# Kernel optimization log

Hardware: AMD Instinct MI355X
Metric: run time of the kernel (lower is better)

The kernel has to match this reference:

```python
import jax, jax.numpy as jnp
import numpy as np

S_VIEWS = 7  # sampled_view from init


def _select_idx(F0, s_views):
    # F0: [B, N, C]; returns idx: [B, s_views] int32 view indices
    B, N, C = F0.shape
    # argmax over views per channel (torch.max(F0,1)[1]) -> [B, C], values in [0, N)
    f_max = jnp.argmax(F0, axis=1)
    # bounded histogram over the N view bins (replaces torch.unique(..., return_counts=True))
    counts = jnp.zeros((B, N), jnp.int32).at[jnp.arange(B)[:, None], f_max].add(1)
    u = jnp.sum(counts > 0, axis=-1)  # number of unique views per batch, [B]
    # --- topk branch (u >= s_views) ---
    # torch.unique is ascending, so topk-by-count with ascending tie-break ==
    # lax.top_k over the per-bin counts (ties -> lower bin index == smaller view id)
    _, idx_topk = jax.lax.top_k(counts, s_views)  # [B, s_views]
    # --- replication-pad branch (u < s_views) ---
    # sorted unique view ids first, sentinel N for empty bins
    sorted_views = jnp.sort(jnp.where(counts > 0, jnp.arange(N)[None, :], N), axis=-1)
    # left-pad with the smallest unique value: position j maps to max(j-(s-u), 0)
    pad_pos = jnp.maximum(jnp.arange(s_views)[None, :] - (s_views - u[:, None]), 0)
    idx_pad = jnp.take_along_axis(sorted_views, pad_pos, axis=-1)  # [B, s_views]
    return jnp.where((u < s_views)[:, None], idx_pad, idx_topk).astype(jnp.int32)


def setup_inputs() -> dict:
    key = jax.random.key(0)
    k1, k2 = jax.random.split(key)
    B, N, C = 256, 20, 4096
    F0 = jax.random.normal(k1, (B, N, C), dtype=jnp.float32)
    vertices0 = jax.random.normal(k2, (B, N, 3), dtype=jnp.float32)
    return {"F0": F0, "vertices0": vertices0, "k": 7}


def reference(F0, vertices0, k):
    idx = _select_idx(F0, S_VIEWS)  # [B, s_views]
    F_new = jnp.take_along_axis(F0, idx[:, :, None], axis=1)          # [B, s_views, C]
    vertices_new = jnp.take_along_axis(vertices0, idx[:, :, None], axis=1)  # [B, s_views, 3]
    return (F_new, vertices_new)
```

## Files before the change

### kernel.cpp

```cpp
#include <hip/hip_runtime.h>

#define BATCHES  256
#define NVIEWS   20
#define CHANNELS 4096
#define KSEL     7
#define NT       1024

__global__ __launch_bounds__(NT) void view_select_kernel(
    const float* __restrict__ F0,
    const float* __restrict__ V0,
    float* __restrict__ out)
{
    const int b = blockIdx.x;
    const int t = threadIdx.x;

    __shared__ int counts[NVIEWS];
    __shared__ int sidx[KSEL];

    if (t < NVIEWS) counts[t] = 0;
    __syncthreads();

    const float* Fb = F0 + (size_t)b * NVIEWS * CHANNELS;
    const float4* Fb4 = (const float4*)Fb;

    float4 best = Fb4[t];
    int bi0 = 0, bi1 = 0, bi2 = 0, bi3 = 0;
    #pragma unroll
    for (int n = 1; n < NVIEWS; ++n) {
        float4 v = Fb4[(size_t)n * (CHANNELS/4) + t];
        if (v.x > best.x) { best.x = v.x; bi0 = n; }
        if (v.y > best.y) { best.y = v.y; bi1 = n; }
        if (v.z > best.z) { best.z = v.z; bi2 = n; }
        if (v.w > best.w) { best.w = v.w; bi3 = n; }
    }
    atomicAdd(&counts[bi0], 1);
    atomicAdd(&counts[bi1], 1);
    atomicAdd(&counts[bi2], 1);
    atomicAdd(&counts[bi3], 1);
    __syncthreads();

    if (t == 0) {
        int u = 0;
        #pragma unroll
        for (int n = 0; n < NVIEWS; ++n) u += (counts[n] > 0) ? 1 : 0;

        if (u >= KSEL) {
            int c[NVIEWS];
            #pragma unroll
            for (int n = 0; n < NVIEWS; ++n) c[n] = counts[n];
            for (int j = 0; j < KSEL; ++j) {
                int bestn = 0, bestc = c[0];
                for (int n = 1; n < NVIEWS; ++n)
                    if (c[n] > bestc) { bestc = c[n]; bestn = n; }
                sidx[j] = bestn;
                c[bestn] = -1;
            }
        } else {
            int uniq[NVIEWS]; int m = 0;
            for (int n = 0; n < NVIEWS; ++n)
                if (counts[n] > 0) uniq[m++] = n;
            for (int j = 0; j < KSEL; ++j) {
                int p = j - (KSEL - u);
                if (p < 0) p = 0;
                sidx[j] = uniq[p];
            }
        }
    }
    __syncthreads();

    float4* out4 = (float4*)out;
    const size_t ob = (size_t)b * KSEL * (CHANNELS/4);
    #pragma unroll
    for (int j = 0; j < KSEL; ++j) {
        int iv = sidx[j];
        out4[ob + (size_t)j * (CHANNELS/4) + t] =
            Fb4[(size_t)iv * (CHANNELS/4) + t];
    }

    const size_t F_OUT = (size_t)BATCHES * KSEL * CHANNELS;
    if (t < KSEL * 3) {
        int j = t / 3;
        out[F_OUT + (size_t)b * KSEL * 3 + t] =
            V0[(size_t)b * NVIEWS * 3 + (size_t)sidx[j] * 3 + (t % 3)];
    }
}

extern "C" void kernel_launch(void* const* d_in, const int* in_sizes, int n_in,
                              void* d_out, int out_size, void* d_ws, size_t ws_size,
                              hipStream_t stream) {
    const float* F0 = (const float*)d_in[0];
    const float* V0 = (const float*)d_in[1];
    float* out = (float*)d_out;

    view_select_kernel<<<BATCHES, NT, 0, stream>>>(F0, V0, out);
}
```

Measured before the change: 26.14 us.

## Keep all views in registers, per-wave histograms, gather from registers

Loads all 20 view vectors into registers up front so the argmax pass issues every load at once. The same registers then serve the output copy, which avoids re-reading the selected views from global memory. The shared-memory histogram is split into per-wave bins that are reduced afterwards to cut atomic contention. The cost is 80 VGPRs of float data per thread at 1024 threads per block, which risks spilling and lower occupancy, plus a select chain for the gather.

Result: slower. 37.20 us (+42.3%).

```diff
diff --git a/kernel.cpp b/kernel.cpp
--- a/kernel.cpp
+++ b/kernel.cpp
@@ -5,38 +5,52 @@
 #define CHANNELS 4096
 #define KSEL     7
 #define NT       1024
+#define NWAVES   (NT / 64)
 
 __global__ __launch_bounds__(NT) void view_select_kernel(
     const float* __restrict__ F0,
     const float* __restrict__ V0,
     float* __restrict__ out)
 {
-    const int b = blockIdx.x;
-    const int t = threadIdx.x;
+    const int b    = blockIdx.x;
+    const int t    = threadIdx.x;
+    const int wave = t >> 6;
+    const int lane = t & 63;
 
+    __shared__ int wh[NWAVES][NVIEWS];
     __shared__ int counts[NVIEWS];
     __shared__ int sidx[KSEL];
 
-    if (t < NVIEWS) counts[t] = 0;
-    __syncthreads();
+    if (lane < NVIEWS) wh[wave][lane] = 0;
 
-    const float* Fb = F0 + (size_t)b * NVIEWS * CHANNELS;
-    const float4* Fb4 = (const float4*)Fb;
+    const float4* Fb4 = (const float4*)(F0 + (size_t)b * NVIEWS * CHANNELS);
 
-    float4 best = Fb4[t];
+    float4 v[NVIEWS];
+    #pragma unroll
+    for (int n = 0; n < NVIEWS; ++n)
+        v[n] = Fb4[(size_t)n * (CHANNELS / 4) + t];
+
+    float4 best = v[0];
     int bi0 = 0, bi1 = 0, bi2 = 0, bi3 = 0;
     #pragma unroll
     for (int n = 1; n < NVIEWS; ++n) {
-        float4 v = Fb4[(size_t)n * (CHANNELS/4) + t];
-        if (v.x > best.x) { best.x = v.x; bi0 = n; }
-        if (v.y > best.y) { best.y = v.y; bi1 = n; }
-        if (v.z > best.z) { best.z = v.z; bi2 = n; }
-        if (v.w > best.w) { best.w = v.w; bi3 = n; }
+        if (v[n].x > best.x) { best.x = v[n].x; bi0 = n; }
+        if (v[n].y > best.y) { best.y = v[n].y; bi1 = n; }
+        if (v[n].z > best.z) { best.z = v[n].z; bi2 = n; }
+        if (v[n].w > best.w) { best.w = v[n].w; bi3 = n; }
     }
-    atomicAdd(&counts[bi0], 1);
-    atomicAdd(&counts[bi1], 1);
-    atomicAdd(&counts[bi2], 1);
-    atomicAdd(&counts[bi3], 1);
+    atomicAdd(&wh[wave][bi0], 1);
+    atomicAdd(&wh[wave][bi1], 1);
+    atomicAdd(&wh[wave][bi2], 1);
+    atomicAdd(&wh[wave][bi3], 1);
+    __syncthreads();
+
+    if (t < NVIEWS) {
+        int s = 0;
+        #pragma unroll
+        for (int w = 0; w < NWAVES; ++w) s += wh[w][t];
+        counts[t] = s;
+    }
     __syncthreads();
 
     if (t == 0) {
@@ -69,12 +83,15 @@
     __syncthreads();
 
     float4* out4 = (float4*)out;
-    const size_t ob = (size_t)b * KSEL * (CHANNELS/4);
+    const size_t ob = (size_t)b * KSEL * (CHANNELS / 4);
     #pragma unroll
     for (int j = 0; j < KSEL; ++j) {
-        int iv = sidx[j];
-        out4[ob + (size_t)j * (CHANNELS/4) + t] =
-            Fb4[(size_t)iv * (CHANNELS/4) + t];
+        int iv = __builtin_amdgcn_readfirstlane(sidx[j]);
+        float4 r = v[0];
+        #pragma unroll
+        for (int n = 1; n < NVIEWS; ++n)
+            if (iv == n) r = v[n];
+        out4[ob + (size_t)j * (CHANNELS / 4) + t] = r;
     }
 
     const size_t F_OUT = (size_t)BATCHES * KSEL * CHANNELS;
```

## Split view selection into parallel histogram and gather kernels

Applied to the files above, without the earlier changes.

The single kernel, one block per batch, becomes two kernels. The first splits each batch's channels across four blocks and builds per-wave LDS histograms, writing partial counts to workspace. The second launches one block per (batch, selected view); each block recomputes the top-k selection from the partial counts and copies one row. This raises grid size and parallelism, at the cost of an extra launch, a workspace round trip, and re-reading the selected F0 rows in a separate pass.

After: 31.55 us. 20.7% more time.

```diff
diff --git a/kernel.cpp b/kernel.cpp
--- a/kernel.cpp
+++ b/kernel.cpp
@@ -4,84 +4,103 @@
 #define NVIEWS   20
 #define CHANNELS 4096
 #define KSEL     7
-#define NT       1024
+#define CHUNKS   (CHANNELS / 4)
+#define QSPLIT   4
+#define NT1      256
+#define CPB      (CHUNKS / QSPLIT)
 
-__global__ __launch_bounds__(NT) void view_select_kernel(
+__global__ __launch_bounds__(NT1) void hist_kernel(
     const float* __restrict__ F0,
-    const float* __restrict__ V0,
-    float* __restrict__ out)
+    int* __restrict__ partial)
 {
-    const int b = blockIdx.x;
+    const int q = blockIdx.x;
+    const int b = blockIdx.y;
     const int t = threadIdx.x;
+    const int wave = t >> 6, lane = t & 63;
 
-    __shared__ int counts[NVIEWS];
-    __shared__ int sidx[KSEL];
+    __shared__ int wh[NT1 / 64][NVIEWS];
+    if (lane < NVIEWS) wh[wave][lane] = 0;
 
-    if (t < NVIEWS) counts[t] = 0;
-    __syncthreads();
+    const float4* Fb4 = (const float4*)(F0 + (size_t)b * NVIEWS * CHANNELS);
+    const int c = q * CPB + t;
 
-    const float* Fb = F0 + (size_t)b * NVIEWS * CHANNELS;
-    const float4* Fb4 = (const float4*)Fb;
-
-    float4 best = Fb4[t];
+    float4 best = Fb4[c];
     int bi0 = 0, bi1 = 0, bi2 = 0, bi3 = 0;
     #pragma unroll
     for (int n = 1; n < NVIEWS; ++n) {
-        float4 v = Fb4[(size_t)n * (CHANNELS/4) + t];
+        float4 v = Fb4[(size_t)n * CHUNKS + c];
         if (v.x > best.x) { best.x = v.x; bi0 = n; }
         if (v.y > best.y) { best.y = v.y; bi1 = n; }
         if (v.z > best.z) { best.z = v.z; bi2 = n; }
         if (v.w > best.w) { best.w = v.w; bi3 = n; }
     }
-    atomicAdd(&counts[bi0], 1);
-    atomicAdd(&counts[bi1], 1);
-    atomicAdd(&counts[bi2], 1);
-    atomicAdd(&counts[bi3], 1);
+    atomicAdd(&wh[wave][bi0], 1);
+    atomicAdd(&wh[wave][bi1], 1);
+    atomicAdd(&wh[wave][bi2], 1);
+    atomicAdd(&wh[wave][bi3], 1);
     __syncthreads();
 
+    if (t < NVIEWS)
+        partial[((size_t)b * QSPLIT + q) * NVIEWS + t] =
+            wh[0][t] + wh[1][t] + wh[2][t] + wh[3][t];
+}
+
+__global__ __launch_bounds__(256) void gather_kernel(
+    const float* __restrict__ F0,
+    const float* __restrict__ V0,
+    const int* __restrict__ partial,
+    float* __restrict__ out)
+{
+    const int j = blockIdx.x;
+    const int b = blockIdx.y;
+    const int t = threadIdx.x;
+
+    __shared__ int s_iv;
+
     if (t == 0) {
+        int counts[NVIEWS];
+        const int* p = partial + (size_t)b * QSPLIT * NVIEWS;
+        #pragma unroll
+        for (int n = 0; n < NVIEWS; ++n)
+            counts[n] = p[n] + p[NVIEWS + n] + p[2 * NVIEWS + n] + p[3 * NVIEWS + n];
+
         int u = 0;
         #pragma unroll
         for (int n = 0; n < NVIEWS; ++n) u += (counts[n] > 0) ? 1 : 0;
 
+        int sidx[KSEL];
         if (u >= KSEL) {
-            int c[NVIEWS];
-            #pragma unroll
-            for (int n = 0; n < NVIEWS; ++n) c[n] = counts[n];
-            for (int j = 0; j < KSEL; ++j) {
-                int bestn = 0, bestc = c[0];
+            for (int jj = 0; jj < KSEL; ++jj) {
+                int bestn = 0, bestc = counts[0];
                 for (int n = 1; n < NVIEWS; ++n)
-                    if (c[n] > bestc) { bestc = c[n]; bestn = n; }
-                sidx[j] = bestn;
-                c[bestn] = -1;
+                    if (counts[n] > bestc) { bestc = counts[n]; bestn = n; }
+                sidx[jj] = bestn;
+                counts[bestn] = -1;
             }
         } else {
             int uniq[NVIEWS]; int m = 0;
             for (int n = 0; n < NVIEWS; ++n)
                 if (counts[n] > 0) uniq[m++] = n;
-            for (int j = 0; j < KSEL; ++j) {
-                int p = j - (KSEL - u);
-                if (p < 0) p = 0;
-                sidx[j] = uniq[p];
+            for (int jj = 0; jj < KSEL; ++jj) {
+                int pp = jj - (KSEL - u);
+                if (pp < 0) pp = 0;
+                sidx[jj] = uniq[pp];
             }
         }
+        s_iv = sidx[j];
     }
     __syncthreads();
+    const int iv = s_iv;
 
-    float4* out4 = (float4*)out;
-    const size_t ob = (size_t)b * KSEL * (CHANNELS/4);
+    const float4* src = (const float4*)(F0 + ((size_t)b * NVIEWS + iv) * CHANNELS);
+    float4* dst = (float4*)out + ((size_t)b * KSEL + j) * CHUNKS;
     #pragma unroll
-    for (int j = 0; j < KSEL; ++j) {
-        int iv = sidx[j];
-        out4[ob + (size_t)j * (CHANNELS/4) + t] =
-            Fb4[(size_t)iv * (CHANNELS/4) + t];
-    }
+    for (int k = 0; k < 4; ++k)
+        dst[t + k * 256] = src[t + k * 256];
 
-    const size_t F_OUT = (size_t)BATCHES * KSEL * CHANNELS;
-    if (t < KSEL * 3) {
-        int j = t / 3;
-        out[F_OUT + (size_t)b * KSEL * 3 + t] =
-            V0[(size_t)b * NVIEWS * 3 + (size_t)sidx[j] * 3 + (t % 3)];
+    if (t < 3) {
+        out[(size_t)BATCHES * KSEL * CHANNELS + ((size_t)b * KSEL + j) * 3 + t] =
+            V0[((size_t)b * NVIEWS + iv) * 3 + t];
     }
 }
 
@@ -91,6 +110,11 @@
     const float* F0 = (const float*)d_in[0];
     const float* V0 = (const float*)d_in[1];
     float* out = (float*)d_out;
+    int* partial = (int*)d_ws;
 
-    view_select_kernel<<<BATCHES, NT, 0, stream>>>(F0, V0, out);
+    dim3 g1(QSPLIT, BATCHES);
+    hist_kernel<<<g1, NT1, 0, stream>>>(F0, partial);
+
+    dim3 g2(KSEL, BATCHES);
+    gather_kernel<<<g2, 256, 0, stream>>>(F0, V0, partial, out);
 }
```
